# Optimization experiments

Hardware: AMD Instinct MI355X
Metric: run time of the kernel (lower is better)

The kernel has to match this reference:

```python
import jax, jax.numpy as jnp
import numpy as np

DN = ('NCHW', 'OIHW', 'NCHW')

def conv(x, w, stride=1, pad=0, groups=1):
    return jax.lax.conv_general_dilated(x, w, (stride, stride), [(pad, pad), (pad, pad)],
                                         dimension_numbers=DN, feature_group_count=groups)

def pw(x, w, b=None):  # 1x1 conv, w: [O, C]
    y = jnp.einsum('bchw,oc->bohw', x, w)
    return y if b is None else y + b[None, :, None, None]

def bn(x, g, b):  # eval-mode BatchNorm2d with running_mean=0, running_var=1 -> affine
    return x * g[None, :, None, None] + b[None, :, None, None]

def gelu(x):
    return jax.nn.gelu(x, approximate=False)

def adaptive_avg_pool(x, K):  # faithful torch AdaptiveAvgPool2d bin edges
    B, C, H, W = x.shape
    rows = []
    for i in range(K):
        hs, he = (i * H) // K, -((-(i + 1) * H) // K)
        cols = []
        for j in range(K):
            ws, we = (j * W) // K, -((-(j + 1) * W) // K)
            cols.append(x[:, :, hs:he, ws:we].mean(axis=(2, 3)))
        rows.append(jnp.stack(cols, axis=-1))
    return jnp.stack(rows, axis=-2)  # [B,C,K,K]

def _forward(x, relative_pos_enc, dc_w, dc_b, dcp1_w, dcp1_g, dcp1_b, dcp2_w, dcp2_b,
             q_w, q_b, kv_w, kv_b, sr1_w, sr1_g, sr1_b, sr2_w, sr2_g, sr2_b,
             lc_w, lc_b, p1_w, p1_b, p1_g, p1_bb, p2_w, p2_b, p2_g, p2_bb,
             p3_w, p3_b, p3_g, p3_bb):
    B, C, H, W = x.shape
    Ch = C // 2
    x1, x2 = x[:, :Ch], x[:, Ch:]

    # ---- DynamicConv2d (local branch) ----
    G, K = dc_w.shape[0], dc_w.shape[-1]
    def dc_proj(z):
        z = gelu(bn(pw(z, dcp1_w), dcp1_g, dcp1_b))
        return pw(z, dcp2_w, dcp2_b)
    scale = dc_proj(adaptive_avg_pool(x1, K)).reshape(B, G, Ch, K, K)
    scale = jax.nn.softmax(scale, axis=1)
    weight = jnp.sum(scale * dc_w[None], axis=1)  # [B,Ch,K,K]
    bscale = dc_proj(x1.mean(axis=(2, 3), keepdims=True)).reshape(B, G, Ch)
    bscale = jax.nn.softmax(bscale, axis=1)
    dyn_bias = jnp.sum(bscale * dc_b[None], axis=1).reshape(-1)  # [B*Ch]
    y1 = conv(x1.reshape(1, B * Ch, H, W), weight.reshape(B * Ch, 1, K, K),
              pad=K // 2, groups=B * Ch)
    y1 = (y1 + dyn_bias[None, :, None, None]).reshape(B, Ch, H, W)

    # ---- Attention (global branch, sr_ratio=4) ----
    heads = relative_pos_enc.shape[1]
    hd = Ch // heads
    sc = hd ** -0.5
    q = pw(x2, q_w, q_b).reshape(B, heads, hd, H * W).transpose(0, 1, 3, 2)  # [B,h,N,hd]
    kv = conv(x2, sr1_w, stride=4, pad=3, groups=Ch)  # depthwise 7x7 stride 4
    kv = gelu(bn(kv, sr1_g, sr1_b))
    kv = bn(kv * sr2_w[None, :, None, None], sr2_g, sr2_b)  # depthwise 1x1 + BN
    kv = conv(kv, lc_w, pad=1, groups=Ch) + lc_b[None, :, None, None] + kv
    kv = pw(kv, kv_w, kv_b)  # [B, 2*Ch, Hk, Wk]
    k, v = kv[:, :Ch], kv[:, Ch:]
    Nk = k.shape[-2] * k.shape[-1]
    k = k.reshape(B, heads, hd, Nk)
    v = v.reshape(B, heads, hd, Nk).transpose(0, 1, 3, 2)  # [B,h,Nk,hd]
    attn = jnp.einsum('bhnd,bhdm->bhnm', q, k) * sc + relative_pos_enc
    attn = jax.nn.softmax(attn, axis=-1)
    y2 = jnp.einsum('bhnm,bhmd->bhnd', attn, v).transpose(0, 1, 3, 2).reshape(B, Ch, H, W)

    # ---- fuse projection + residual ----
    y = jnp.concatenate([y1, y2], axis=1)
    z = conv(y, p1_w, pad=1, groups=C) + p1_b[None, :, None, None]
    z = bn(gelu(z), p1_g, p1_bb)
    z = bn(gelu(pw(z, p2_w, p2_b)), p2_g, p2_bb)
    z = bn(pw(z, p3_w, p3_b), p3_g, p3_bb)
    return z + y


def setup_inputs() -> dict:
    key = jax.random.key(0)
    ks = jax.random.split(key, 40)
    B, C, H, W = 64, 128, 56, 56
    Ch, G, K, heads, inner = C // 2, 2, 3, 2, 16
    N, Nk = H * W, 14 * 14
    p = lambda i, shp: jax.random.normal(ks[i], shp, dtype=jnp.float32) * 0.02
    return {
        'x': jax.random.normal(ks[0], (B, C, H, W), dtype=jnp.float32),
        'relative_pos_enc': p(1, (1, heads, N, Nk)),
        'dc_w': p(2, (G, Ch, K, K)), 'dc_b': p(3, (G, Ch)),
        'dcp1_w': p(4, (Ch // 4, Ch)), 'dcp1_g': 1.0 + p(5, (Ch // 4,)), 'dcp1_b': p(6, (Ch // 4,)),
        'dcp2_w': p(7, (Ch * G, Ch // 4)), 'dcp2_b': p(8, (Ch * G,)),
        'q_w': p(9, (Ch, Ch)), 'q_b': p(10, (Ch,)),
        'kv_w': p(11, (2 * Ch, Ch)), 'kv_b': p(12, (2 * Ch,)),
        'sr1_w': p(13, (Ch, 1, 7, 7)), 'sr1_g': 1.0 + p(14, (Ch,)), 'sr1_b': p(15, (Ch,)),
        'sr2_w': 1.0 + p(16, (Ch,)), 'sr2_g': 1.0 + p(17, (Ch,)), 'sr2_b': p(18, (Ch,)),
        'lc_w': p(19, (Ch, 1, 3, 3)), 'lc_b': p(20, (Ch,)),
        'p1_w': p(21, (C, 1, 3, 3)), 'p1_b': p(22, (C,)), 'p1_g': 1.0 + p(23, (C,)), 'p1_bb': p(24, (C,)),
        'p2_w': p(25, (inner, C)), 'p2_b': p(26, (inner,)), 'p2_g': 1.0 + p(27, (inner,)), 'p2_bb': p(28, (inner,)),
        'p3_w': p(29, (C, inner)), 'p3_b': p(30, (C,)), 'p3_g': 1.0 + p(31, (C,)), 'p3_bb': p(32, (C,)),
    }


def reference(x, relative_pos_enc, dc_w, dc_b, dcp1_w, dcp1_g, dcp1_b, dcp2_w, dcp2_b,
              q_w, q_b, kv_w, kv_b, sr1_w, sr1_g, sr1_b, sr2_w, sr2_g, sr2_b,
              lc_w, lc_b, p1_w, p1_b, p1_g, p1_bb, p2_w, p2_b, p2_g, p2_bb,
              p3_w, p3_b, p3_g, p3_bb):
    return _forward(x, relative_pos_enc, dc_w, dc_b, dcp1_w, dcp1_g, dcp1_b, dcp2_w, dcp2_b,
                    q_w, q_b, kv_w, kv_b, sr1_w, sr1_g, sr1_b, sr2_w, sr2_g, sr2_b,
                    lc_w, lc_b, p1_w, p1_b, p1_g, p1_bb, p2_w, p2_b, p2_g, p2_bb,
                    p3_w, p3_b, p3_g, p3_bb)
```

## Files before the change

kernel.cpp:

```cpp
#include <hip/hip_runtime.h>
#include <cstddef>

#define NPIX 3136

typedef __attribute__((ext_vector_type(8))) short bf16x8;
typedef __attribute__((ext_vector_type(4))) float f32x4;

__device__ __forceinline__ float gelu_f(float x){
  return 0.5f*x*(1.0f+erff(x*0.70710678118654752440f));
}

__device__ __forceinline__ unsigned pack_bf16(float a, float b){
  unsigned ua = __float_as_uint(a), ub = __float_as_uint(b);
  ua = (ua + 0x7FFFu + ((ua>>16)&1u)) >> 16;
  ub = (ub + 0x7FFFu + ((ub>>16)&1u)) >> 16;
  return ua | (ub<<16);
}

__device__ __forceinline__ unsigned cvt_pk_bf16(float a, float b){
  unsigned r;
  asm("v_cvt_pk_bf16_f32 %0, %1, %2" : "=v"(r) : "v"(a), "v"(b));
  return r;
}

__global__ void k_pool(const float* __restrict__ x, float* __restrict__ pooled, float* __restrict__ xmean){
  int b = blockIdx.x >> 6, c = blockIdx.x & 63;
  const float4* xp = (const float4*)(x + ((size_t)(b*128 + c))*NPIX);
  float r[9] = {0,0,0,0,0,0,0,0,0};
  float tot = 0.f;
  for (int p4 = threadIdx.x; p4 < 784; p4 += 64){
    float4 v4 = xp[p4];
    int p = p4*4;
    int h = p/56, w0 = p%56;
    bool h0 = (h<=18), h1 = (h>=18 && h<=37), h2 = (h>=37);
    float vv[4] = {v4.x, v4.y, v4.z, v4.w};
    #pragma unroll
    for (int j=0;j<4;j++){
      int w = w0+j; float v = vv[j];
      tot += v;
      bool b0 = (w<=18), b1 = (w>=18 && w<=37), b2 = (w>=37);
      if(h0){ if(b0) r[0]+=v; if(b1) r[1]+=v; if(b2) r[2]+=v; }
      if(h1){ if(b0) r[3]+=v; if(b1) r[4]+=v; if(b2) r[5]+=v; }
      if(h2){ if(b0) r[6]+=v; if(b1) r[7]+=v; if(b2) r[8]+=v; }
    }
  }
  #pragma unroll
  for (int o=32;o>0;o>>=1){
    #pragma unroll
    for (int k=0;k<9;k++) r[k]+=__shfl_xor(r[k],o);
    tot += __shfl_xor(tot,o);
  }
  if (threadIdx.x==0){
    const float cs[3]={19.f,20.f,19.f};
    #pragma unroll
    for(int i=0;i<3;i++)
      #pragma unroll
      for(int j=0;j<3;j++)
        pooled[(size_t)blockIdx.x*9 + i*3+j] = r[i*3+j]/(cs[i]*cs[j]);
    xmean[blockIdx.x] = tot*(1.f/3136.f);
  }
}

__global__ void k_dcproj(const float* __restrict__ pooled, const float* __restrict__ xmean,
    const float* __restrict__ dcp1_w, const float* __restrict__ dcp1_g, const float* __restrict__ dcp1_b,
    const float* __restrict__ dcp2_w, const float* __restrict__ dcp2_b,
    const float* __restrict__ dc_w, const float* __restrict__ dc_b,
    float* __restrict__ weightO, float* __restrict__ dyn_bias){
  int b = blockIdx.x; int tid = threadIdx.x;
  __shared__ float sp[576], sm[64], t1[144], t1b[16], s2[1152], s2b[128];
  for (int i=tid;i<576;i+=256) sp[i]=pooled[(size_t)b*576+i];
  if (tid<64) sm[tid]=xmean[b*64+tid];
  __syncthreads();
  for (int idx=tid; idx<160; idx+=256){
    if (idx<144){
      int o=idx/9, pos=idx%9; float s=0.f;
      for(int c2=0;c2<64;c2++) s += sp[c2*9+pos]*dcp1_w[o*64+c2];
      t1[idx]=gelu_f(s*dcp1_g[o]+dcp1_b[o]);
    } else {
      int o=idx-144; float s=0.f;
      for(int c2=0;c2<64;c2++) s+=sm[c2]*dcp1_w[o*64+c2];
      t1b[o]=gelu_f(s*dcp1_g[o]+dcp1_b[o]);
    }
  }
  __syncthreads();
  for (int idx=tid; idx<1280; idx+=256){
    if (idx<1152){
      int o=idx/9,pos=idx%9; float s=dcp2_b[o];
      #pragma unroll
      for(int i=0;i<16;i++) s+=t1[i*9+pos]*dcp2_w[o*16+i];
      s2[idx]=s;
    } else {
      int o=idx-1152; float s=dcp2_b[o];
      #pragma unroll
      for(int i=0;i<16;i++) s+=t1b[i]*dcp2_w[o*16+i];
      s2b[o]=s;
    }
  }
  __syncthreads();
  for (int idx=tid; idx<640; idx+=256){
    if (idx<576){
      int ch=idx/9, pos=idx%9;
      float a=s2[ch*9+pos], bb=s2[(64+ch)*9+pos];
      float m=fmaxf(a,bb); float e0=expf(a-m), e1=expf(bb-m); float w0=e0/(e0+e1);
      weightO[(size_t)b*576+idx] = w0*dc_w[ch*9+pos] + (1.f-w0)*dc_w[576+ch*9+pos];
    } else {
      int ch=idx-576;
      float a=s2b[ch], bb=s2b[64+ch];
      float m=fmaxf(a,bb); float e0=expf(a-m), e1=expf(bb-m); float w0=e0/(e0+e1);
      dyn_bias[b*64+ch] = w0*dc_b[ch] + (1.f-w0)*dc_b[64+ch];
    }
  }
}

__global__ void k_y1(const float* __restrict__ x, const float* __restrict__ weightO,
                     const float* __restrict__ dyn_bias, float* __restrict__ y){
  __shared__ float pl[NPIX];
  const float4* xp4 = (const float4*)(x + ((size_t)(blockIdx.x>>6)*128 + (blockIdx.x&63))*NPIX);
  float4* pl4 = (float4*)pl;
  for (int i=threadIdx.x;i<784;i+=256) pl4[i]=xp4[i];
  float w9[9];
  #pragma unroll
  for (int k=0;k<9;k++) w9[k]=weightO[(size_t)blockIdx.x*9+k];
  float bias = dyn_bias[blockIdx.x];
  __syncthreads();
  float* yp = y + ((size_t)(blockIdx.x>>6)*128 + (blockIdx.x&63))*NPIX;
  for (int p4=threadIdx.x;p4<784;p4+=256){
    int h=p4/14, w0=(p4%14)*4;
    float o4[4];
    #pragma unroll
    for (int j=0;j<4;j++){
      int w=w0+j; float acc=bias;
      #pragma unroll
      for (int i=0;i<3;i++){ int hh=h+i-1; if((unsigned)hh<56u){
        #pragma unroll
        for(int jj=0;jj<3;jj++){ int ww=w+jj-1; if((unsigned)ww<56u) acc += pl[hh*56+ww]*w9[i*3+jj]; } } }
      o4[j]=acc;
    }
    float4 res = {o4[0],o4[1],o4[2],o4[3]};
    *(float4*)(yp + h*56 + w0) = res;
  }
}

__global__ void k_qproj(const float* __restrict__ x, const float* __restrict__ q_w,
                        const float* __restrict__ q_b, unsigned* __restrict__ qbf){
  int b = blockIdx.x/49, t = blockIdx.x%49; int n0 = t*64; int tid = threadIdx.x;
  __shared__ float qwT[64*64];
  __shared__ float xt[64*64];
  for (int i4=tid; i4<1024; i4+=256){ int o=i4>>4, c4=(i4&15)*4;
    float4 w4 = *(const float4*)(q_w + o*64 + c4);
    qwT[(c4+0)*64+o]=w4.x; qwT[(c4+1)*64+o]=w4.y; qwT[(c4+2)*64+o]=w4.z; qwT[(c4+3)*64+o]=w4.w; }
  for (int i4=tid; i4<1024; i4+=256){ int c2=i4>>4, p4=(i4&15)*4;
    float4 v4 = *(const float4*)(x + ((size_t)(b*128+64+c2))*NPIX + n0 + p4);
    *(float4*)(xt + c2*64 + p4) = v4; }
  __syncthreads();
  int d2_ = tid&31, prow = tid>>5;
  int o0 = 2*d2_; int h = d2_>>4, dd = d2_&15;
  float b0 = q_b[o0], b1 = q_b[o0+1];
  float a0[8], a1[8];
  #pragma unroll
  for (int i=0;i<8;i++){ a0[i]=b0; a1[i]=b1; }
  #pragma unroll 4
  for (int c2=0;c2<64;c2++){
    float w0 = qwT[c2*64+o0], w1 = qwT[c2*64+o0+1];
    #pragma unroll
    for (int i=0;i<8;i++){ float xv = xt[c2*64 + prow*8 + i]; a0[i]+=xv*w0; a1[i]+=xv*w1; }
  }
  const float sc = 0.17677669529663687f;
  #pragma unroll
  for (int i=0;i<8;i++)
    qbf[((size_t)(b*2+h)*NPIX + n0 + prow*8 + i)*16 + dd] = pack_bf16(a0[i]*sc, a1[i]*sc);
}

__global__ void k_sr(const float* __restrict__ x, const float* __restrict__ sr1_w,
                     const float* __restrict__ sr1_g, const float* __restrict__ sr1_b,
                     const float* __restrict__ sr2_w, const float* __restrict__ sr2_g,
                     const float* __restrict__ sr2_b, float* __restrict__ kv2){
  int b=blockIdx.x>>6, c=blockIdx.x&63;
  __shared__ float pl[NPIX];
  const float4* xp4 = (const float4*)(x + ((size_t)(b*128+64+c))*NPIX);
  float4* pl4 = (float4*)pl;
  for (int i=threadIdx.x;i<784;i+=256) pl4[i]=xp4[i];
  __syncthreads();
  int t=threadIdx.x;
  if (t<196){
    int oy=t/14, ox=t%14;
    float acc=0.f;
    #pragma unroll
    for(int i=0;i<7;i++){ int yy=oy*4-3+i; if((unsigned)yy<56u){
      #pragma unroll
      for(int j=0;j<7;j++){ int xx=ox*4-3+j; if((unsigned)xx<56u) acc += pl[yy*56+xx]*sr1_w[c*49+i*7+j]; } } }
    float g = gelu_f(acc*sr1_g[c]+sr1_b[c]);
    kv2[(size_t)blockIdx.x*196+t] = (g*sr2_w[c])*sr2_g[c]+sr2_b[c];
  }
}

__global__ void k_lc(const float* __restrict__ kv2, const float* __restrict__ lc_w,
                     const float* __restrict__ lc_b, float* __restrict__ kv3){
  int c=blockIdx.x&63;
  __shared__ float pl[196];
  for (int p=threadIdx.x;p<196;p+=256) pl[p]=kv2[(size_t)blockIdx.x*196+p];
  __syncthreads();
  int t=threadIdx.x;
  if (t<196){
    int oy=t/14, ox=t%14; float acc=lc_b[c]+pl[t];
    #pragma unroll
    for(int i=0;i<3;i++){int yy=oy+i-1; if((unsigned)yy<14u){
      #pragma unroll
      for(int j=0;j<3;j++){int xx=ox+j-1; if((unsigned)xx<14u) acc+=pl[yy*14+xx]*lc_w[c*9+i*3+j];}}}
    kv3[(size_t)blockIdx.x*196+t]=acc;
  }
}

__global__ void k_kv(const float* __restrict__ kv3, const float* __restrict__ kv_w,
                     const float* __restrict__ kv_b, unsigned* __restrict__ kbf,
                     unsigned* __restrict__ vbf){
  __shared__ float s[64*28];
  __shared__ float wl[64*64];
  int bid = blockIdx.x;
  int b = bid/14, rem = bid%14;
  int half = rem/7, mc = rem%7;
  int m0 = mc*28;
  int tid = threadIdx.x;
  for (int i=tid;i<1792;i+=256){ int c=i/28, j=i%28;
    s[i] = kv3[((size_t)(b*64)+c)*196 + m0 + j]; }
  for (int j=tid;j<1024;j+=256)
    ((float4*)wl)[j] = ((const float4*)(kv_w + half*4096))[j];
  __syncthreads();
  if (half==0){
    for (int idx=tid; idx<896; idx+=256){
      int mloc = idx%28, o2 = idx/28; int m = m0 + mloc; int o = 2*o2;
      float acc0=kv_b[o], acc1=kv_b[o+1];
      #pragma unroll 8
      for (int c2=0;c2<64;c2++){ float v=s[c2*28+mloc];
        acc0+=v*wl[o*64+c2]; acc1+=v*wl[(o+1)*64+c2]; }
      int h=o2>>4, d2=o2&15;
      kbf[((size_t)(b*2+h)*208 + m)*16 + d2] = pack_bf16(acc0, acc1);
    }
    if (mc==6){
      for (int i=tid;i<384;i+=256){ int h=i/192, r=i%192, m=196+(r>>4), d2=r&15;
        kbf[((size_t)(b*2+h)*208 + m)*16 + d2] = 0; }
    }
  } else {
    for (int idx=tid; idx<896; idx+=256){
      int vo = idx/14, m2l = idx%14; int m2 = mc*14 + m2l; int m = 2*m2;
      int o = 64+vo; int mloc = m - m0;
      float acc0=kv_b[o], acc1=kv_b[o];
      #pragma unroll 8
      for (int c2=0;c2<64;c2++){ float w=wl[vo*64+c2];
        acc0+=s[c2*28+mloc]*w; acc1+=s[c2*28+mloc+1]*w; }
      int h=vo>>5, d=vo&31, dh=d>>4, dd=d&15;
      int s_=m>>5, rm=m&31, g=rm>>3, ip=(rm&7)>>1;
      vbf[(((size_t)(b*2+h)*14 + dh*7 + s_)*64 + g*16 + dd)*4 + ip] = pack_bf16(acc0, acc1);
    }
    if (mc==6){
      for (int idx=tid; idx<896; idx+=256){
        int vo = idx/14, m2l = idx%14; int m = 2*(98+m2l);
        int h=vo>>5, d=vo&31, dh=d>>4, dd=d&15;
        int s_=m>>5, rm=m&31, g=rm>>3, ip=(rm&7)>>1;
        vbf[(((size_t)(b*2+h)*14 + dh*7 + s_)*64 + g*16 + dd)*4 + ip] = 0;
      }
    }
  }
}

__global__ __launch_bounds__(256,4) void k_attn(const unsigned* __restrict__ qbf,
                       const unsigned* __restrict__ kbf, const unsigned* __restrict__ vbf,
                       const float* __restrict__ rpe, float* __restrict__ y){
  __shared__ unsigned SMEM[4*16*116];
  int bh = blockIdx.x & 127, tile = blockIdx.x >> 7;
  int b=bh>>1, h=bh&1, n0=tile*64, tid=threadIdx.x;
  int wv = tid>>6, l = tid&63, g = l>>4, c = l&15, qr = wv*16;

  bf16x8 qa = *(const bf16x8*)(qbf + ((size_t)bh*NPIX + n0+qr+c)*16 + 4*g);

  const float* rp = rpe + ((size_t)(h*NPIX + n0 + qr))*196;
  f32x4 acc[13];
  #pragma unroll
  for (int mt=0; mt<12; mt++){
    #pragma unroll
    for (int r=0;r<4;r++) acc[mt][r] = rp[(size_t)(4*g+r)*196 + mt*16 + c];
  }
  {
    bool v = (c<4);
    #pragma unroll
    for (int r=0;r<4;r++) acc[12][r] = v ? rp[(size_t)(4*g+r)*196 + 192 + c] : -1e30f;
  }
  const unsigned* kB = kbf + (size_t)bh*208*16;
  #pragma unroll
  for (int mt=0; mt<13; mt++){
    bf16x8 kb = *(const bf16x8*)(kB + ((size_t)(mt*16 + c))*16 + 4*g);
    acc[mt] = __builtin_amdgcn_mfma_f32_16x16x32_bf16(qa, kb, acc[mt], 0,0,0);
  }
  float inv[4];
  #pragma unroll
  for (int r=0;r<4;r++){
    float sm = 0.f;
    #pragma unroll
    for (int mt=0;mt<13;mt++){ float e = __expf(acc[mt][r]); acc[mt][r]=e; sm += e; }
    #pragma unroll
    for (int o=1;o<16;o<<=1) sm += __shfl_xor(sm,o);
    inv[r] = 1.f/sm;
  }
  unsigned* Pw = SMEM + wv*1856;
  #pragma unroll
  for (int mt=0;mt<13;mt++){
    #pragma unroll
    for (int r=0;r<4;r++){
      float other = __shfl_xor(acc[mt][r], 1);
      unsigned pk = cvt_pk_bf16(acc[mt][r], other);
      if ((l&1)==0) Pw[(4*g+r)*116 + mt*8 + (c>>1)] = pk;
    }
  }
  #pragma unroll
  for (int i=0;i<2;i++){ int row=(l>>3)+8*i, cc=l&7; Pw[row*116 + 104 + cc] = 0; }
  const short* PsS = (const short*)Pw;
  const unsigned* vB = vbf + (size_t)bh*3584;
  f32x4 o0 = {0.f,0.f,0.f,0.f}, o1 = {0.f,0.f,0.f,0.f};
  #pragma unroll
  for (int s=0;s<7;s++){
    bf16x8 pa = *(const bf16x8*)(PsS + c*232 + s*32 + 8*g);
    bf16x8 v0 = *(const bf16x8*)(vB + ((size_t)(s*64 + l))*4);
    bf16x8 v1 = *(const bf16x8*)(vB + ((size_t)((7+s)*64 + l))*4);
    o0 = __builtin_amdgcn_mfma_f32_16x16x32_bf16(pa, v0, o0, 0,0,0);
    o1 = __builtin_amdgcn_mfma_f32_16x16x32_bf16(pa, v1, o1, 0,0,0);
  }
  __syncthreads();
  float* Os = (float*)SMEM;
  #pragma unroll
  for (int r=0;r<4;r++){
    Os[(qr + 4*g + r)*33 + c]      = o0[r]*inv[r];
    Os[(qr + 4*g + r)*33 + 16 + c] = o1[r]*inv[r];
  }
  __syncthreads();
  size_t base = ((size_t)(b*128 + 64 + h*32))*NPIX;
  for (int i=tid;i<2048;i+=256){ int d=i>>6, rr=i&63;
    y[base + (size_t)d*NPIX + n0 + rr] = Os[rr*33 + d]; }
}

__global__ void k_p1(const float* __restrict__ y, const float* __restrict__ p1_w,
                     const float* __restrict__ p1_b, const float* __restrict__ p1_g,
                     const float* __restrict__ p1_bb, unsigned* __restrict__ z1p){
  __shared__ float YS[2*NPIX];
  int b = blockIdx.x>>6, cp = blockIdx.x&63;
  int c0 = 2*cp;
  int tid = threadIdx.x;
  const float4* yp0 = (const float4*)(y + ((size_t)(b*128+c0))*NPIX);
  const float4* yp1 = (const float4*)(y + ((size_t)(b*128+c0+1))*NPIX);
  float4* YS4 = (float4*)YS;
  for (int i=tid;i<784;i+=256){ YS4[i]=yp0[i]; YS4[784+i]=yp1[i]; }
  float pw_a[9], pw_b[9];
  #pragma unroll
  for (int k=0;k<9;k++){ pw_a[k]=p1_w[c0*9+k]; pw_b[k]=p1_w[(c0+1)*9+k]; }
  float pbA=p1_b[c0], pgA=p1_g[c0], pbbA=p1_bb[c0];
  float pbB=p1_b[c0+1], pgB=p1_g[c0+1], pbbB=p1_bb[c0+1];
  __syncthreads();
  unsigned* zp = z1p + ((size_t)(b*64+cp))*NPIX;
  for (int p4=tid;p4<784;p4+=256){
    int h=p4/14, w0=(p4%14)*4;
    unsigned pk[4];
    #pragma unroll
    for (int j=0;j<4;j++){
      int w=w0+j; float aA=pbA, aB=pbB;
      #pragma unroll
      for (int i=0;i<3;i++){ int hh=h+i-1; if((unsigned)hh<56u){
        #pragma unroll
        for(int jj=0;jj<3;jj++){ int ww=w+jj-1; if((unsigned)ww<56u){
          aA += YS[hh*56+ww]*pw_a[i*3+jj];
          aB += YS[NPIX+hh*56+ww]*pw_b[i*3+jj]; } } } }
      pk[j] = pack_bf16(gelu_f(aA)*pgA+pbbA, gelu_f(aB)*pgB+pbbB);
    }
    uint4 res = {pk[0],pk[1],pk[2],pk[3]};
    *(uint4*)(zp + h*56 + w0) = res;
  }
}

__global__ __launch_bounds__(256) void k_p23m(const unsigned* __restrict__ z1p, const float* __restrict__ y,
                      const float* __restrict__ p2_w, const float* __restrict__ p2_b,
                      const float* __restrict__ p2_g, const float* __restrict__ p2_bb,
                      const float* __restrict__ p3_w, const float* __restrict__ p3_b,
                      const float* __restrict__ p3_g, const float* __restrict__ p3_bb,
                      float* __restrict__ out){
  __shared__ unsigned W2F[4*64*4];
  __shared__ unsigned W3F[8*64*4];
  __shared__ unsigned T16[4][16*12];
  int tid = threadIdx.x;
  for (int j=tid;j<1024;j+=256){
    int s=j>>8, ll=(j>>2)&63, e2=j&3;
    int i=ll&15, c=32*s+8*(ll>>4)+2*e2;
    W2F[j] = pack_bf16(p2_w[i*128+c], p2_w[i*128+c+1]);
  }
  for (int j=tid;j<2048;j+=256){
    int grp=j>>8, ll=(j>>2)&63, e2=j&3;
    int gg=ll>>4, o=grp*16+(ll&15);
    unsigned v=0u;
    if (gg<2){ int k=8*gg+2*e2; float g3=p3_g[o];
      v = pack_bf16(p3_w[o*16+k]*g3, p3_w[o*16+k+1]*g3); }
    W3F[j]=v;
  }
  __syncthreads();
  int w = tid>>6, l = tid&63, g = l>>4, li = l&15;
  int b = blockIdx.x/49, t = blockIdx.x%49;
  int px0 = t*64 + w*16;
  int px = px0 + li;
  const unsigned* zb = z1p + ((size_t)(b*64))*NPIX + px;
  float pb = p2_b[li];
  f32x4 acc; acc[0]=pb; acc[1]=pb; acc[2]=pb; acc[3]=pb;
  #pragma unroll
  for (int s=0;s<4;s++){
    union { unsigned u[4]; bf16x8 v; } A;
    int slot0 = 16*s + 4*g;
    #pragma unroll
    for (int j=0;j<4;j++) A.u[j] = zb[(size_t)(slot0+j)*NPIX];
    bf16x8 Bf = *(const bf16x8*)(W2F + (s*64 + l)*4);
    acc = __builtin_amdgcn_mfma_f32_16x16x32_bf16(A.v, Bf, acc, 0,0,0);
  }
  float g2v = p2_g[li], bb2 = p2_bb[li];
  unsigned* tw = &T16[w][0];
  #pragma unroll
  for (int r=0;r<4;r++){
    float tv = gelu_f(acc[r])*g2v + bb2;
    float other = __shfl_xor(tv, 1);
    unsigned pk = cvt_pk_bf16(tv, other);
    if ((l&1)==0) tw[(4*g + r)*12 + (li>>1)] = pk;
  }
  bf16x8 Af3 = {0,0,0,0,0,0,0,0};
  if (g<2){
    union { unsigned u[4]; bf16x8 v; } T;
    const unsigned* tr = tw + li*12 + 4*g;
    T.u[0]=tr[0]; T.u[1]=tr[1]; T.u[2]=tr[2]; T.u[3]=tr[3];
    Af3 = T.v;
  }
  #pragma unroll
  for (int grp=0; grp<8; grp++){
    int o = grp*16 + li;
    float b3 = p3_b[o]*p3_g[o] + p3_bb[o];
    size_t rowoff = ((size_t)(b*128+o))*NPIX + px0 + 4*g;
    float4 yv = *(const float4*)(y + rowoff);
    f32x4 c2; c2[0]=yv.x+b3; c2[1]=yv.y+b3; c2[2]=yv.z+b3; c2[3]=yv.w+b3;
    bf16x8 Bf3 = *(const bf16x8*)(W3F + (grp*64+l)*4);
    c2 = __builtin_amdgcn_mfma_f32_16x16x32_bf16(Af3, Bf3, c2, 0,0,0);
    float4 res = {c2[0],c2[1],c2[2],c2[3]};
    *(float4*)(out + rowoff) = res;
  }
}

extern "C" void kernel_launch(void* const* d_in, const int* in_sizes, int n_in,
                              void* d_out, int out_size, void* d_ws, size_t ws_size,
                              hipStream_t stream) {
  (void)in_sizes; (void)n_in; (void)out_size; (void)ws_size;
  const float* x       = (const float*)d_in[0];
  const float* rpe     = (const float*)d_in[1];
  const float* dc_w    = (const float*)d_in[2];
  const float* dc_b    = (const float*)d_in[3];
  const float* dcp1_w  = (const float*)d_in[4];
  const float* dcp1_g  = (const float*)d_in[5];
  const float* dcp1_b  = (const float*)d_in[6];
  const float* dcp2_w  = (const float*)d_in[7];
  const float* dcp2_b  = (const float*)d_in[8];
  const float* q_w     = (const float*)d_in[9];
  const float* q_b     = (const float*)d_in[10];
  const float* kv_w    = (const float*)d_in[11];
  const float* kv_b    = (const float*)d_in[12];
  const float* sr1_w   = (const float*)d_in[13];
  const float* sr1_g   = (const float*)d_in[14];
  const float* sr1_b   = (const float*)d_in[15];
  const float* sr2_w   = (const float*)d_in[16];
  const float* sr2_g   = (const float*)d_in[17];
  const float* sr2_b   = (const float*)d_in[18];
  const float* lc_w    = (const float*)d_in[19];
  const float* lc_b    = (const float*)d_in[20];
  const float* p1_w    = (const float*)d_in[21];
  const float* p1_b    = (const float*)d_in[22];
  const float* p1_g    = (const float*)d_in[23];
  const float* p1_bb   = (const float*)d_in[24];
  const float* p2_w    = (const float*)d_in[25];
  const float* p2_b    = (const float*)d_in[26];
  const float* p2_g    = (const float*)d_in[27];
  const float* p2_bb   = (const float*)d_in[28];
  const float* p3_w    = (const float*)d_in[29];
  const float* p3_b    = (const float*)d_in[30];
  const float* p3_g    = (const float*)d_in[31];
  const float* p3_bb   = (const float*)d_in[32];
  float* out = (float*)d_out;
  float* ws  = (float*)d_ws;

  const size_t OFF_Y     = 0;
  const size_t OFF_A     = 25690112;
  const size_t OFF_Z1P   = 25690112 + 6422528;
  const size_t OFF_POOL  = 54591488;
  const size_t OFF_XMEAN = 54628352;
  const size_t OFF_W     = 54632448;
  const size_t OFF_DB    = 54669312;
  const size_t OFF_KV2   = 54673408;
  const size_t OFF_KV3   = 55476224;
  const size_t OFF_K     = 56279040;
  const size_t OFF_V     = 57081856;

  float*    yb    = ws + OFF_Y;
  unsigned* qbf   = (unsigned*)(ws + OFF_A);
  unsigned* z1p   = (unsigned*)(ws + OFF_Z1P);
  float*    pool  = ws + OFF_POOL;
  float*    xmean = ws + OFF_XMEAN;
  float*    wgt   = ws + OFF_W;
  float*    dbias = ws + OFF_DB;
  float*    kv2   = ws + OFF_KV2;
  float*    kv3   = ws + OFF_KV3;
  unsigned* kbf   = (unsigned*)(ws + OFF_K);
  unsigned* vbf   = (unsigned*)(ws + OFF_V);

  k_pool  <<<4096, 64, 0, stream>>>(x, pool, xmean);
  k_dcproj<<<64, 256, 0, stream>>>(pool, xmean, dcp1_w, dcp1_g, dcp1_b, dcp2_w, dcp2_b, dc_w, dc_b, wgt, dbias);
  k_y1    <<<4096, 256, 0, stream>>>(x, wgt, dbias, yb);
  k_qproj <<<3136, 256, 0, stream>>>(x, q_w, q_b, qbf);
  k_sr    <<<4096, 256, 0, stream>>>(x, sr1_w, sr1_g, sr1_b, sr2_w, sr2_g, sr2_b, kv2);
  k_lc    <<<4096, 256, 0, stream>>>(kv2, lc_w, lc_b, kv3);
  k_kv    <<<896, 256, 0, stream>>>(kv3, kv_w, kv_b, kbf, vbf);
  k_attn  <<<6272, 256, 0, stream>>>(qbf, kbf, vbf, rpe, yb);
  k_p1    <<<4096, 256, 0, stream>>>(yb, p1_w, p1_b, p1_g, p1_bb, z1p);
  k_p23m  <<<3136, 256, 0, stream>>>(z1p, yb, p2_w, p2_b, p2_g, p2_bb, p3_w, p3_b, p3_g, p3_bb, out);
}
```

Measured before the change: 295.3 us.

## Store intermediate y tensor as packed bf16 channel pairs

The concatenated intermediate y (local conv output and attention output) is now stored as bf16, with two adjacent channels packed per 32-bit word. k_y1 processes two channels per block, and k_attn packs its output pairs. k_p1 and k_p23m unpack on read. This halves the memory traffic for writing and reading y across four kernels, but lowers the precision of the residual path and the depthwise conv input.

```diff
diff --git a/kernel.cpp b/kernel.cpp
--- a/kernel.cpp
+++ b/kernel.cpp
@@ -22,6 +22,9 @@
   asm("v_cvt_pk_bf16_f32 %0, %1, %2" : "=v"(r) : "v"(a), "v"(b));
   return r;
 }
+
+__device__ __forceinline__ float bf16lo(unsigned u){ return __uint_as_float(u<<16); }
+__device__ __forceinline__ float bf16hi(unsigned u){ return __uint_as_float(u & 0xFFFF0000u); }
 
 __global__ void k_pool(const float* __restrict__ x, float* __restrict__ pooled, float* __restrict__ xmean){
   int b = blockIdx.x >> 6, c = blockIdx.x & 63;
@@ -113,31 +116,37 @@
 }
 
 __global__ void k_y1(const float* __restrict__ x, const float* __restrict__ weightO,
-                     const float* __restrict__ dyn_bias, float* __restrict__ y){
-  __shared__ float pl[NPIX];
-  const float4* xp4 = (const float4*)(x + ((size_t)(blockIdx.x>>6)*128 + (blockIdx.x&63))*NPIX);
-  float4* pl4 = (float4*)pl;
-  for (int i=threadIdx.x;i<784;i+=256) pl4[i]=xp4[i];
-  float w9[9];
-  #pragma unroll
-  for (int k=0;k<9;k++) w9[k]=weightO[(size_t)blockIdx.x*9+k];
-  float bias = dyn_bias[blockIdx.x];
-  __syncthreads();
-  float* yp = y + ((size_t)(blockIdx.x>>6)*128 + (blockIdx.x&63))*NPIX;
-  for (int p4=threadIdx.x;p4<784;p4+=256){
+                     const float* __restrict__ dyn_bias, unsigned* __restrict__ ybf){
+  __shared__ float XS[2*NPIX];
+  int b = blockIdx.x>>5, cp = blockIdx.x&31;
+  int c0 = 2*cp;
+  int tid = threadIdx.x;
+  const float4* xp0 = (const float4*)(x + ((size_t)(b*128+c0))*NPIX);
+  const float4* xp1 = (const float4*)(x + ((size_t)(b*128+c0+1))*NPIX);
+  float4* XS4 = (float4*)XS;
+  for (int i=tid;i<784;i+=256){ XS4[i]=xp0[i]; XS4[784+i]=xp1[i]; }
+  float w9a[9], w9b[9];
+  #pragma unroll
+  for (int k=0;k<9;k++){ w9a[k]=weightO[((size_t)(b*64+c0))*9+k]; w9b[k]=weightO[((size_t)(b*64+c0+1))*9+k]; }
+  float biasA = dyn_bias[b*64+c0], biasB = dyn_bias[b*64+c0+1];
+  __syncthreads();
+  unsigned* yp = ybf + ((size_t)(b*64+cp))*NPIX;
+  for (int p4=tid;p4<784;p4+=256){
     int h=p4/14, w0=(p4%14)*4;
-    float o4[4];
+    unsigned pk[4];
     #pragma unroll
     for (int j=0;j<4;j++){
-      int w=w0+j; float acc=bias;
+      int w=w0+j; float aA=biasA, aB=biasB;
       #pragma unroll
       for (int i=0;i<3;i++){ int hh=h+i-1; if((unsigned)hh<56u){
         #pragma unroll
-        for(int jj=0;jj<3;jj++){ int ww=w+jj-1; if((unsigned)ww<56u) acc += pl[hh*56+ww]*w9[i*3+jj]; } } }
-      o4[j]=acc;
-    }
-    float4 res = {o4[0],o4[1],o4[2],o4[3]};
-    *(float4*)(yp + h*56 + w0) = res;
+        for(int jj=0;jj<3;jj++){ int ww=w+jj-1; if((unsigned)ww<56u){
+          aA += XS[hh*56+ww]*w9a[i*3+jj];
+          aB += XS[NPIX+hh*56+ww]*w9b[i*3+jj]; } } } }
+      pk[j] = pack_bf16(aA, aB);
+    }
+    uint4 res = {pk[0],pk[1],pk[2],pk[3]};
+    *(uint4*)(yp + h*56 + w0) = res;
   }
 }
 
@@ -265,7 +274,7 @@
 
 __global__ __launch_bounds__(256,4) void k_attn(const unsigned* __restrict__ qbf,
                        const unsigned* __restrict__ kbf, const unsigned* __restrict__ vbf,
-                       const float* __restrict__ rpe, float* __restrict__ y){
+                       const float* __restrict__ rpe, unsigned* __restrict__ ybf){
   __shared__ unsigned SMEM[4*16*116];
   int bh = blockIdx.x & 127, tile = blockIdx.x >> 7;
   int b=bh>>1, h=bh&1, n0=tile*64, tid=threadIdx.x;
@@ -332,22 +341,28 @@
     Os[(qr + 4*g + r)*33 + 16 + c] = o1[r]*inv[r];
   }
   __syncthreads();
-  size_t base = ((size_t)(b*128 + 64 + h*32))*NPIX;
-  for (int i=tid;i<2048;i+=256){ int d=i>>6, rr=i&63;
-    y[base + (size_t)d*NPIX + n0 + rr] = Os[rr*33 + d]; }
-}
-
-__global__ void k_p1(const float* __restrict__ y, const float* __restrict__ p1_w,
+  size_t base = ((size_t)(b*64 + 32 + h*16))*NPIX;
+  for (int i=tid;i<1024;i+=256){ int d2=i>>6, rr=i&63;
+    unsigned pk = cvt_pk_bf16(Os[rr*33 + 2*d2], Os[rr*33 + 2*d2 + 1]);
+    ybf[base + (size_t)d2*NPIX + n0 + rr] = pk; }
+}
+
+__global__ void k_p1(const unsigned* __restrict__ ybf, const float* __restrict__ p1_w,
                      const float* __restrict__ p1_b, const float* __restrict__ p1_g,
                      const float* __restrict__ p1_bb, unsigned* __restrict__ z1p){
   __shared__ float YS[2*NPIX];
   int b = blockIdx.x>>6, cp = blockIdx.x&63;
   int c0 = 2*cp;
   int tid = threadIdx.x;
-  const float4* yp0 = (const float4*)(y + ((size_t)(b*128+c0))*NPIX);
-  const float4* yp1 = (const float4*)(y + ((size_t)(b*128+c0+1))*NPIX);
-  float4* YS4 = (float4*)YS;
-  for (int i=tid;i<784;i+=256){ YS4[i]=yp0[i]; YS4[784+i]=yp1[i]; }
+  const uint4* yp4 = (const uint4*)(ybf + ((size_t)(b*64+cp))*NPIX);
+  for (int i=tid;i<784;i+=256){
+    uint4 v = yp4[i];
+    int p = i*4;
+    YS[p+0]=bf16lo(v.x); YS[NPIX+p+0]=bf16hi(v.x);
+    YS[p+1]=bf16lo(v.y); YS[NPIX+p+1]=bf16hi(v.y);
+    YS[p+2]=bf16lo(v.z); YS[NPIX+p+2]=bf16hi(v.z);
+    YS[p+3]=bf16lo(v.w); YS[NPIX+p+3]=bf16hi(v.w);
+  }
   float pw_a[9], pw_b[9];
   #pragma unroll
   for (int k=0;k<9;k++){ pw_a[k]=p1_w[c0*9+k]; pw_b[k]=p1_w[(c0+1)*9+k]; }
@@ -374,7 +389,7 @@
   }
 }
 
-__global__ __launch_bounds__(256) void k_p23m(const unsigned* __restrict__ z1p, const float* __restrict__ y,
+__global__ __launch_bounds__(256) void k_p23m(const unsigned* __restrict__ z1p, const unsigned* __restrict__ ybf,
                       const float* __restrict__ p2_w, const float* __restrict__ p2_b,
                       const float* __restrict__ p2_g, const float* __restrict__ p2_bb,
                       const float* __restrict__ p3_w, const float* __restrict__ p3_b,
@@ -430,17 +445,21 @@
     T.u[0]=tr[0]; T.u[1]=tr[1]; T.u[2]=tr[2]; T.u[3]=tr[3];
     Af3 = T.v;
   }
+  int par = li & 1;
   #pragma unroll
   for (int grp=0; grp<8; grp++){
     int o = grp*16 + li;
     float b3 = p3_b[o]*p3_g[o] + p3_bb[o];
-    size_t rowoff = ((size_t)(b*128+o))*NPIX + px0 + 4*g;
-    float4 yv = *(const float4*)(y + rowoff);
-    f32x4 c2; c2[0]=yv.x+b3; c2[1]=yv.y+b3; c2[2]=yv.z+b3; c2[3]=yv.w+b3;
+    size_t poff = ((size_t)(b*64 + (o>>1)))*NPIX + px0 + 4*g;
+    uint4 yv4 = *(const uint4*)(ybf + poff);
+    float y0,y1,y2,y3;
+    if (par){ y0=bf16hi(yv4.x); y1=bf16hi(yv4.y); y2=bf16hi(yv4.z); y3=bf16hi(yv4.w); }
+    else    { y0=bf16lo(yv4.x); y1=bf16lo(yv4.y); y2=bf16lo(yv4.z); y3=bf16lo(yv4.w); }
+    f32x4 c2; c2[0]=y0+b3; c2[1]=y1+b3; c2[2]=y2+b3; c2[3]=y3+b3;
     bf16x8 Bf3 = *(const bf16x8*)(W3F + (grp*64+l)*4);
     c2 = __builtin_amdgcn_mfma_f32_16x16x32_bf16(Af3, Bf3, c2, 0,0,0);
     float4 res = {c2[0],c2[1],c2[2],c2[3]};
-    *(float4*)(out + rowoff) = res;
+    *(float4*)(out + ((size_t)(b*128+o))*NPIX + px0 + 4*g) = res;
   }
 }
 
@@ -496,7 +515,7 @@
   const size_t OFF_K     = 56279040;
   const size_t OFF_V     = 57081856;
 
-  float*    yb    = ws + OFF_Y;
+  unsigned* ybf   = (unsigned*)(ws + OFF_Y);
   unsigned* qbf   = (unsigned*)(ws + OFF_A);
   unsigned* z1p   = (unsigned*)(ws + OFF_Z1P);
   float*    pool  = ws + OFF_POOL;
@@ -510,12 +529,12 @@
 
   k_pool  <<<4096, 64, 0, stream>>>(x, pool, xmean);
   k_dcproj<<<64, 256, 0, stream>>>(pool, xmean, dcp1_w, dcp1_g, dcp1_b, dcp2_w, dcp2_b, dc_w, dc_b, wgt, dbias);
-  k_y1    <<<4096, 256, 0, stream>>>(x, wgt, dbias, yb);
+  k_y1    <<<2048, 256, 0, stream>>>(x, wgt, dbias, ybf);
   k_qproj <<<3136, 256, 0, stream>>>(x, q_w, q_b, qbf);
   k_sr    <<<4096, 256, 0, stream>>>(x, sr1_w, sr1_g, sr1_b, sr2_w, sr2_g, sr2_b, kv2);
   k_lc    <<<4096, 256, 0, stream>>>(kv2, lc_w, lc_b, kv3);
   k_kv    <<<896, 256, 0, stream>>>(kv3, kv_w, kv_b, kbf, vbf);
-  k_attn  <<<6272, 256, 0, stream>>>(qbf, kbf, vbf, rpe, yb);
-  k_p1    <<<4096, 256, 0, stream>>>(yb, p1_w, p1_b, p1_g, p1_bb, z1p);
-  k_p23m  <<<3136, 256, 0, stream>>>(z1p, yb, p2_w, p2_b, p2_g, p2_bb, p3_w, p3_b, p3_g, p3_bb, out);
-}
+  k_attn  <<<6272, 256, 0, stream>>>(qbf, kbf, vbf, rpe, ybf);
+  k_p1    <<<4096, 256, 0, stream>>>(ybf, p1_w, p1_b, p1_g, p1_bb, z1p);
+  k_p23m  <<<3136, 256, 0, stream>>>(z1p, ybf, p2_w, p2_b, p2_g, p2_bb, p3_w, p3_b, p3_g, p3_bb, out);
+}
```

Result: faster. 275.4 us (-6.7%).
